# Performance work log

Hardware: AMD Instinct MI355X
Metric: run time of the kernel (lower is better)

## Reference

```python
import jax, jax.numpy as jnp
import numpy as np

# Static configuration (from init_kwargs)
SPLIT_SEC = (128, 320, 320)   # (n_nucl_species..., n_up, n_dn)
N = sum(SPLIT_SEC)            # 768 particles
N_NUCL = sum(SPLIT_SEC[:-2])  # 128
N_DN = SPLIT_SEC[-1]          # 320
SINGLE = 256
PAIR = 64
D_FEAT = SINGLE + len(SPLIT_SEC) * PAIR + len(SPLIT_SEC) * SINGLE  # 1216
SQRT2 = 1.4142135623730951
GELU_RESCALE = 1.7128586      # fvmc rescaled-gelu constant (unit output variance)

_SPLIT_IDX = np.cumsum(SPLIT_SEC)[:-1]

def _pair_type():
    pt = np.zeros((N, N), np.int32)
    sn, se = slice(0, N_NUCL), slice(N_NUCL, N)
    su = slice(N_NUCL, N_NUCL + SPLIT_SEC[-2])
    sd = slice(N_NUCL + SPLIT_SEC[-2], N)
    pt[sn, se] = pt[se, sn] = 1
    pt[su, su] = pt[sd, sd] = 2
    pt[su, sd] = pt[sd, su] = 3
    return pt

PAIR_TYPE = _pair_type()  # static int mask, values in {0,1,2,3}

def actv(x):
    # parse_activation('gelu', rescale=True)
    return jax.nn.gelu(x) * GELU_RESCALE

def residual(x, y):
    # adaptive_residual with rescale=True (shapes always match here)
    return (x + y) / SQRT2

def aggregate_features(h1, h2):
    # per-section mean of h1 over particles -> (n_sec, d1), tiled to (N, n_sec, d1)
    h1_mean = jnp.stack([s.mean(axis=0) for s in jnp.split(h1, _SPLIT_IDX, axis=0)], axis=0)
    h1_mean = jnp.tile(h1_mean[None], (N, 1, 1))
    # per-section mean of h2 over axis 1 -> (N, n_sec, d2)
    h2_mean = jnp.stack([s.mean(axis=1) for s in jnp.split(h2, _SPLIT_IDX, axis=1)], axis=-2)
    # spin symmetry: swap the last two (up/dn) mean channels for the dn rows
    h1_sw = jnp.stack([h1_mean[-N_DN:, -1], h1_mean[-N_DN:, -2]], axis=1)
    h1_mean = h1_mean.at[-N_DN:, -2:].set(h1_sw)
    h2_sw = jnp.stack([h2_mean[-N_DN:, -1], h2_mean[-N_DN:, -2]], axis=1)
    h2_mean = h2_mean.at[-N_DN:, -2:].set(h2_sw)
    return jnp.concatenate([h1, h2_mean.reshape(N, -1), h1_mean.reshape(N, -1)], axis=-1)

def setup_inputs() -> dict:
    key = jax.random.key(0)
    ks = jax.random.split(key, 5)
    sc = lambda fan_in: 1.0 / np.sqrt(fan_in)  # lecun-normal-ish scale
    return {
        "h1": jax.random.normal(ks[0], (N, SINGLE), jnp.float32),
        "h2": jax.random.normal(ks[1], (N, N, PAIR), jnp.float32),
        "W1n": jax.random.normal(ks[2], (D_FEAT, SINGLE), jnp.float32) * sc(D_FEAT),
        "b1n": jnp.zeros((SINGLE,), jnp.float32),
        "W1e": jax.random.normal(ks[3], (D_FEAT, SINGLE), jnp.float32) * sc(D_FEAT),
        "b1e": jnp.zeros((SINGLE,), jnp.float32),
        "W2": jax.random.normal(ks[4], (4, PAIR, PAIR), jnp.float32) * sc(PAIR),
        "b2": jnp.zeros((4, PAIR), jnp.float32),
    }

def reference(h1, h2, W1n, b1n, W1e, b1e, W2, b2):
    feats = aggregate_features(h1, h2)  # (N, D_FEAT)
    # h1 update: separate Dense for nuclei vs electrons
    h1_new = jnp.concatenate([
        feats[:N_NUCL] @ W1n + b1n,
        feats[N_NUCL:] @ W1e + b1e,
    ], axis=0)
    h1_out = residual(h1, actv(h1_new))
    # h2 update: per pair-type Dense, masked scatter back (4 static types)
    pt = jnp.asarray(PAIR_TYPE)
    h2_new = jnp.zeros((N, N, PAIR), h2.dtype)
    for p in range(4):
        mask = (pt == p)[..., None]
        h2_new = h2_new + mask * (jnp.einsum('nmd,de->nme', h2, W2[p]) + b2[p])
    h2_out = residual(h2, actv(h2_new))
    return h1_out, h2_out
```

## Files before the change

### kernel.cpp

```cpp
#include <hip/hip_runtime.h>


#define H1OUT_ELEMS (768 * 256)

typedef short short8 __attribute__((ext_vector_type(8)));
typedef float f32x4 __attribute__((ext_vector_type(4)));

__device__ __forceinline__ unsigned short f2bf(float f) {
    unsigned u = __builtin_bit_cast(unsigned, f);
    unsigned r = u + 0x7fffu + ((u >> 16) & 1u);
    return (unsigned short)(r >> 16);
}

__device__ __forceinline__ float gelu_res(float x, float hv) {
    float x2 = x * x;
    float z = x * fmaf(-0.1029432196f, x2, -2.3025850930f);
    float e = __builtin_amdgcn_exp2f(z);
    float r = __builtin_amdgcn_rcpf(1.f + e);
    return fmaf(x * r, 1.2111740f, hv * 0.70710678f);
}

__global__ __launch_bounds__(256) void k_h2pre(
    const float* __restrict__ h2, const float* __restrict__ W2,
    const float* __restrict__ b2, const float* __restrict__ h1,
    const float* __restrict__ W1n, const float* __restrict__ W1e,
    float* __restrict__ out2, float* __restrict__ part2,
    float* __restrict__ part1, unsigned short* __restrict__ WT) {
    __shared__ union SM {
        struct {
            unsigned short A16[64][72];
            unsigned short BT[64][72];
            float          red[16][68];
        } g;
        float tile[64][65];
    } sm;

    int b = blockIdx.x;
    const int t = threadIdx.x;

    if (b < 12) {
        float s = 0.f;
        #pragma unroll 8
        for (int r = 0; r < 64; ++r) s += h1[(size_t)(b * 64 + r) * 256 + t];
        part1[b * 256 + t] = s;
        return;
    }
    if (b < 164) {
        int idx = b - 12;
        int mtx = idx / 76;
        int r2  = idx % 76;
        int k0 = (r2 / 4) * 64, e0 = (r2 % 4) * 64;
        const float* W = mtx ? W1e : W1n;
        #pragma unroll
        for (int i = 0; i < 16; ++i) {
            int j = i * 256 + t;
            int kr = j >> 6, ec = j & 63;
            sm.tile[kr][ec] = W[(size_t)(k0 + kr) * 256 + e0 + ec];
        }
        __syncthreads();
        #pragma unroll
        for (int i = 0; i < 16; ++i) {
            int j = i * 256 + t;
            int er = j >> 6, kc = j & 63;
            WT[((size_t)mtx * 256 + e0 + er) * 1216 + k0 + kc] = f2bf(sm.tile[kc][er]);
        }
        return;
    }

    b -= 164;
    const int ct = b % 12;
    const int n  = b / 12;
    const int m0 = ct * 64;

    const int rs = (n < 128) ? 0 : ((n < 448) ? 1 : 2);
    const int cs = (ct < 2) ? 0 : ((ct < 7) ? 1 : 2);
    int p;
    if (rs == 0)      p = (cs == 0) ? 0 : 1;
    else if (rs == 1) p = (cs == 0) ? 1 : ((cs == 1) ? 2 : 3);
    else              p = (cs == 0) ? 1 : ((cs == 1) ? 3 : 2);

    const float* src = h2 + ((size_t)n * 768 + m0) * 64;
    const int row0 = t >> 4, c4 = (t & 15) << 2;

    float4 v0 = *reinterpret_cast<const float4*>(src + (row0 +  0) * 64 + c4);
    float4 v1 = *reinterpret_cast<const float4*>(src + (row0 + 16) * 64 + c4);
    float4 v2 = *reinterpret_cast<const float4*>(src + (row0 + 32) * 64 + c4);
    float4 v3 = *reinterpret_cast<const float4*>(src + (row0 + 48) * 64 + c4);

    {
        ushort4 bv;
        bv.x = f2bf(v0.x); bv.y = f2bf(v0.y); bv.z = f2bf(v0.z); bv.w = f2bf(v0.w);
        *reinterpret_cast<ushort4*>(&sm.g.A16[row0][c4]) = bv;
        bv.x = f2bf(v1.x); bv.y = f2bf(v1.y); bv.z = f2bf(v1.z); bv.w = f2bf(v1.w);
        *reinterpret_cast<ushort4*>(&sm.g.A16[row0 + 16][c4]) = bv;
        bv.x = f2bf(v2.x); bv.y = f2bf(v2.y); bv.z = f2bf(v2.z); bv.w = f2bf(v2.w);
        *reinterpret_cast<ushort4*>(&sm.g.A16[row0 + 32][c4]) = bv;
        bv.x = f2bf(v3.x); bv.y = f2bf(v3.y); bv.z = f2bf(v3.z); bv.w = f2bf(v3.w);
        *reinterpret_cast<ushort4*>(&sm.g.A16[row0 + 48][c4]) = bv;
    }
    {
        float4 cs4;
        cs4.x = v0.x + v1.x + v2.x + v3.x;
        cs4.y = v0.y + v1.y + v2.y + v3.y;
        cs4.z = v0.z + v1.z + v2.z + v3.z;
        cs4.w = v0.w + v1.w + v2.w + v3.w;
        *reinterpret_cast<float4*>(&sm.g.red[row0][c4]) = cs4;
    }
    const float* w = W2 + p * 4096;
    #pragma unroll
    for (int i = 0; i < 16; ++i) {
        int idx = i * 256 + t;
        int d = idx >> 6, e = idx & 63;
        sm.g.BT[e][d] = f2bf(w[idx]);
    }
    __syncthreads();

    const int lane = t & 63;
    const int wv = t >> 6;

    if (wv == 0) {
        float s = 0.f;
        #pragma unroll
        for (int r = 0; r < 16; ++r) s += sm.g.red[r][lane];
        part2[((size_t)n * 12 + ct) * 64 + lane] = s;
    }

    const int wm = wv >> 1, we = wv & 1;
    const int lr = lane & 15;
    const int lk = lane >> 4;

    f32x4 acc[2][2] = {};
    #pragma unroll
    for (int kh = 0; kh < 2; ++kh) {
        short8 aF[2], bF[2];
        int k = kh * 32 + lk * 8;
        #pragma unroll
        for (int fm = 0; fm < 2; ++fm)
            aF[fm] = *reinterpret_cast<const short8*>(&sm.g.A16[wm * 32 + fm * 16 + lr][k]);
        #pragma unroll
        for (int fe = 0; fe < 2; ++fe)
            bF[fe] = *reinterpret_cast<const short8*>(&sm.g.BT[we * 32 + fe * 16 + lr][k]);
        #pragma unroll
        for (int fm = 0; fm < 2; ++fm)
            #pragma unroll
            for (int fe = 0; fe < 2; ++fe)
                acc[fm][fe] = __builtin_amdgcn_mfma_f32_16x16x32_bf16(
                    aF[fm], bF[fe], acc[fm][fe], 0, 0, 0);
    }

    float* dst = out2 + ((size_t)n * 768 + m0) * 64;
    #pragma unroll
    for (int fm = 0; fm < 2; ++fm) {
        #pragma unroll
        for (int fe = 0; fe < 2; ++fe) {
            int e = we * 32 + fe * 16 + lr;
            float bias = b2[p * 64 + e];
            #pragma unroll
            for (int r = 0; r < 4; ++r) {
                int m = wm * 32 + fm * 16 + lk * 4 + r;
                float hv = src[m * 64 + e];
                float o = gelu_res(acc[fm][fe][r] + bias, hv);
                __builtin_nontemporal_store(o, dst + m * 64 + e);
            }
        }
    }
}

__global__ __launch_bounds__(256) void k_h1f(
    const float* __restrict__ h1, const unsigned short* __restrict__ WT,
    const float* __restrict__ part2, const float* __restrict__ part1,
    const float* __restrict__ b1n, const float* __restrict__ b1e,
    float* __restrict__ out1) {
    __shared__ unsigned short FL[16][1224];

    const int n0 = blockIdx.x * 16;
    const int half = blockIdx.y;
    const int t = threadIdx.x;
    const bool dn = (n0 >= 448);
    const bool nucl = (n0 < 128);

    #pragma unroll
    for (int i = 0; i < 16; ++i) {
        int idx = i * 256 + t;
        int r = idx >> 8, c = idx & 255;
        FL[r][c] = f2bf(h1[(size_t)(n0 + r) * 256 + c]);
    }
    #pragma unroll
    for (int i = 0; i < 12; ++i) {
        int idx = i * 256 + t;
        int r = idx / 192, c = idx % 192;
        int sec = c >> 6, d = c & 63;
        int s2 = (dn && sec >= 1) ? (3 - sec) : sec;
        const float* pr = part2 + (size_t)(n0 + r) * 768;
        float s;
        if (s2 == 0) {
            s = (pr[d] + pr[64 + d]) * (1.f / 128.f);
        } else {
            int q0 = (s2 == 1) ? 2 : 7;
            s = 0.f;
            #pragma unroll
            for (int q = 0; q < 5; ++q) s += pr[(q0 + q) * 64 + d];
            s *= (1.f / 320.f);
        }
        FL[r][256 + c] = f2bf(s);
    }
    #pragma unroll
    for (int i = 0; i < 3; ++i) {
        int j = i * 256 + t;
        int sec = j >> 8, e2 = j & 255;
        int s2 = (dn && sec >= 1) ? (3 - sec) : sec;
        float s;
        if (s2 == 0) {
            s = (part1[e2] + part1[256 + e2]) * (1.f / 128.f);
        } else {
            int q0 = (s2 == 1) ? 2 : 7;
            s = 0.f;
            #pragma unroll
            for (int q = 0; q < 5; ++q) s += part1[(q0 + q) * 256 + e2];
            s *= (1.f / 320.f);
        }
        unsigned short bv = f2bf(s);
        #pragma unroll
        for (int r = 0; r < 16; ++r) FL[r][448 + j] = bv;
    }
    __syncthreads();

    const int w = t >> 6, lane = t & 63;
    const int lr = lane & 15, lk = lane >> 4;
    const int e0 = half * 128 + w * 32;
    const unsigned short* BT = WT + (nucl ? 0 : (size_t)256 * 1216);
    const unsigned short* br0 = BT + (size_t)(e0 + lr) * 1216 + lk * 8;
    const unsigned short* br1 = br0 + (size_t)16 * 1216;
    const unsigned short* ar = &FL[lr][lk * 8];

    f32x4 acc0 = {}, acc1 = {};
    #pragma unroll 2
    for (int k = 0; k < 1216; k += 32) {
        short8 aF = *reinterpret_cast<const short8*>(ar + k);
        short8 b0 = *reinterpret_cast<const short8*>(br0 + k);
        short8 b1 = *reinterpret_cast<const short8*>(br1 + k);
        acc0 = __builtin_amdgcn_mfma_f32_16x16x32_bf16(aF, b0, acc0, 0, 0, 0);
        acc1 = __builtin_amdgcn_mfma_f32_16x16x32_bf16(aF, b1, acc1, 0, 0, 0);
    }

    const float* bb = nucl ? b1n : b1e;
    #pragma unroll
    for (int j = 0; j < 2; ++j) {
        const f32x4 a = j ? acc1 : acc0;
        int e = e0 + j * 16 + lr;
        float bias = bb[e];
        #pragma unroll
        for (int r = 0; r < 4; ++r) {
            int m = n0 + lk * 4 + r;
            float hv = h1[(size_t)m * 256 + e];
            out1[(size_t)m * 256 + e] = gelu_res(a[r] + bias, hv);
        }
    }
}

extern "C" void kernel_launch(void* const* d_in, const int* in_sizes, int n_in,
                              void* d_out, int out_size, void* d_ws, size_t ws_size,
                              hipStream_t stream) {
    const float* h1  = (const float*)d_in[0];
    const float* h2  = (const float*)d_in[1];
    const float* W1n = (const float*)d_in[2];
    const float* b1n = (const float*)d_in[3];
    const float* W1e = (const float*)d_in[4];
    const float* b1e = (const float*)d_in[5];
    const float* W2  = (const float*)d_in[6];
    const float* b2  = (const float*)d_in[7];

    float* out1 = (float*)d_out;
    float* out2 = out1 + H1OUT_ELEMS;

    float* part2 = (float*)d_ws;
    float* part1 = part2 + 768 * 12 * 64;
    unsigned short* WT = (unsigned short*)(part1 + 12 * 256);

    k_h2pre<<<dim3(164 + 12 * 768), 256, 0, stream>>>(
        h2, W2, b2, h1, W1n, W1e, out2, part2, part1, WT);
    k_h1f<<<dim3(48, 2), 256, 0, stream>>>(h1, WT, part2, part1, b1n, b1e, out1);
}
```

Measured before the change: 86.28 us.

## Load MFMA fragments directly from global memory and vectorize weight transpose

The h2 tile blocks no longer stage h2 and W2 through LDS as bf16. Each wave reads its MFMA A and B fragments straight from global memory and converts them to bf16 in registers, and LDS is kept only for the column-sum reduction, which now runs after the MFMA. The W1 transpose blocks switch to 64x32 tiles with 16-byte vectorized bf16 stores, which doubles the number of those blocks. This cuts LDS use and moves the barrier later, at the cost of redundant global loads: each A fragment is loaded by two waves and each W2 fragment is gathered with strided scalar loads in every block.

```diff
diff --git a/kernel.cpp b/kernel.cpp
--- a/kernel.cpp
+++ b/kernel.cpp
@@ -27,12 +27,8 @@
     float* __restrict__ out2, float* __restrict__ part2,
     float* __restrict__ part1, unsigned short* __restrict__ WT) {
     __shared__ union SM {
-        struct {
-            unsigned short A16[64][72];
-            unsigned short BT[64][72];
-            float          red[16][68];
-        } g;
-        float tile[64][65];
+        float red[2][16][68];
+        float tile2[64][33];
     } sm;
 
     int b = blockIdx.x;
@@ -45,29 +41,29 @@
         part1[b * 256 + t] = s;
         return;
     }
-    if (b < 164) {
+    if (b < 316) {
         int idx = b - 12;
-        int mtx = idx / 76;
-        int r2  = idx % 76;
-        int k0 = (r2 / 4) * 64, e0 = (r2 % 4) * 64;
+        int mtx = idx / 152;
+        int r2  = idx % 152;
+        int k0 = (r2 >> 3) * 64, e0 = (r2 & 7) * 32;
         const float* W = mtx ? W1e : W1n;
         #pragma unroll
-        for (int i = 0; i < 16; ++i) {
+        for (int i = 0; i < 8; ++i) {
             int j = i * 256 + t;
-            int kr = j >> 6, ec = j & 63;
-            sm.tile[kr][ec] = W[(size_t)(k0 + kr) * 256 + e0 + ec];
+            int kr = j >> 5, ec = j & 31;
+            sm.tile2[kr][ec] = W[(size_t)(k0 + kr) * 256 + e0 + ec];
         }
         __syncthreads();
-        #pragma unroll
-        for (int i = 0; i < 16; ++i) {
-            int j = i * 256 + t;
-            int er = j >> 6, kc = j & 63;
-            WT[((size_t)mtx * 256 + e0 + er) * 1216 + k0 + kc] = f2bf(sm.tile[kc][er]);
-        }
+        int er = t >> 3, k8 = (t & 7) * 8;
+        short8 o;
+        #pragma unroll
+        for (int j = 0; j < 8; ++j) o[j] = (short)f2bf(sm.tile2[k8 + j][er]);
+        *reinterpret_cast<short8*>(
+            &WT[((size_t)mtx * 256 + e0 + er) * 1216 + k0 + k8]) = o;
         return;
     }
 
-    b -= 164;
+    b -= 316;
     const int ct = b % 12;
     const int n  = b / 12;
     const int m0 = ct * 64;
@@ -80,72 +76,86 @@
     else              p = (cs == 0) ? 1 : ((cs == 1) ? 3 : 2);
 
     const float* src = h2 + ((size_t)n * 768 + m0) * 64;
-    const int row0 = t >> 4, c4 = (t & 15) << 2;
-
-    float4 v0 = *reinterpret_cast<const float4*>(src + (row0 +  0) * 64 + c4);
-    float4 v1 = *reinterpret_cast<const float4*>(src + (row0 + 16) * 64 + c4);
-    float4 v2 = *reinterpret_cast<const float4*>(src + (row0 + 32) * 64 + c4);
-    float4 v3 = *reinterpret_cast<const float4*>(src + (row0 + 48) * 64 + c4);
-
-    {
-        ushort4 bv;
-        bv.x = f2bf(v0.x); bv.y = f2bf(v0.y); bv.z = f2bf(v0.z); bv.w = f2bf(v0.w);
-        *reinterpret_cast<ushort4*>(&sm.g.A16[row0][c4]) = bv;
-        bv.x = f2bf(v1.x); bv.y = f2bf(v1.y); bv.z = f2bf(v1.z); bv.w = f2bf(v1.w);
-        *reinterpret_cast<ushort4*>(&sm.g.A16[row0 + 16][c4]) = bv;
-        bv.x = f2bf(v2.x); bv.y = f2bf(v2.y); bv.z = f2bf(v2.z); bv.w = f2bf(v2.w);
-        *reinterpret_cast<ushort4*>(&sm.g.A16[row0 + 32][c4]) = bv;
-        bv.x = f2bf(v3.x); bv.y = f2bf(v3.y); bv.z = f2bf(v3.z); bv.w = f2bf(v3.w);
-        *reinterpret_cast<ushort4*>(&sm.g.A16[row0 + 48][c4]) = bv;
-    }
-    {
-        float4 cs4;
-        cs4.x = v0.x + v1.x + v2.x + v3.x;
-        cs4.y = v0.y + v1.y + v2.y + v3.y;
-        cs4.z = v0.z + v1.z + v2.z + v3.z;
-        cs4.w = v0.w + v1.w + v2.w + v3.w;
-        *reinterpret_cast<float4*>(&sm.g.red[row0][c4]) = cs4;
-    }
-    const float* w = W2 + p * 4096;
-    #pragma unroll
-    for (int i = 0; i < 16; ++i) {
-        int idx = i * 256 + t;
-        int d = idx >> 6, e = idx & 63;
-        sm.g.BT[e][d] = f2bf(w[idx]);
-    }
-    __syncthreads();
-
     const int lane = t & 63;
     const int wv = t >> 6;
-
-    if (wv == 0) {
-        float s = 0.f;
-        #pragma unroll
-        for (int r = 0; r < 16; ++r) s += sm.g.red[r][lane];
-        part2[((size_t)n * 12 + ct) * 64 + lane] = s;
-    }
-
     const int wm = wv >> 1, we = wv & 1;
-    const int lr = lane & 15;
-    const int lk = lane >> 4;
+    const int lr = lane & 15, lk = lane >> 4;
+
+    const float* arow = src + (wm * 32 + lr) * 64 + lk * 8;
+    float4 af[2][2][2];
+    #pragma unroll
+    for (int fm = 0; fm < 2; ++fm)
+        #pragma unroll
+        for (int kh = 0; kh < 2; ++kh) {
+            const float* pp = arow + fm * 1024 + kh * 32;
+            af[fm][kh][0] = *reinterpret_cast<const float4*>(pp);
+            af[fm][kh][1] = *reinterpret_cast<const float4*>(pp + 4);
+        }
+
+    if (we == 0) {
+        #pragma unroll
+        for (int kh = 0; kh < 2; ++kh) {
+            float4 s0, s1;
+            s0.x = af[0][kh][0].x + af[1][kh][0].x;
+            s0.y = af[0][kh][0].y + af[1][kh][0].y;
+            s0.z = af[0][kh][0].z + af[1][kh][0].z;
+            s0.w = af[0][kh][0].w + af[1][kh][0].w;
+            s1.x = af[0][kh][1].x + af[1][kh][1].x;
+            s1.y = af[0][kh][1].y + af[1][kh][1].y;
+            s1.z = af[0][kh][1].z + af[1][kh][1].z;
+            s1.w = af[0][kh][1].w + af[1][kh][1].w;
+            *reinterpret_cast<float4*>(&sm.red[wm][lr][kh * 32 + lk * 8]) = s0;
+            *reinterpret_cast<float4*>(&sm.red[wm][lr][kh * 32 + lk * 8 + 4]) = s1;
+        }
+    }
+
+    short8 aF[2][2];
+    #pragma unroll
+    for (int fm = 0; fm < 2; ++fm)
+        #pragma unroll
+        for (int kh = 0; kh < 2; ++kh) {
+            short8 o;
+            o[0] = (short)f2bf(af[fm][kh][0].x);
+            o[1] = (short)f2bf(af[fm][kh][0].y);
+            o[2] = (short)f2bf(af[fm][kh][0].z);
+            o[3] = (short)f2bf(af[fm][kh][0].w);
+            o[4] = (short)f2bf(af[fm][kh][1].x);
+            o[5] = (short)f2bf(af[fm][kh][1].y);
+            o[6] = (short)f2bf(af[fm][kh][1].z);
+            o[7] = (short)f2bf(af[fm][kh][1].w);
+            aF[fm][kh] = o;
+        }
+
+    const float* wp = W2 + p * 4096 + we * 32 + lr;
+    short8 bF[2][2];
+    #pragma unroll
+    for (int fe = 0; fe < 2; ++fe)
+        #pragma unroll
+        for (int kh = 0; kh < 2; ++kh) {
+            const float* q = wp + fe * 16 + (kh * 32 + lk * 8) * 64;
+            short8 o;
+            #pragma unroll
+            for (int j = 0; j < 8; ++j) o[j] = (short)f2bf(q[j * 64]);
+            bF[fe][kh] = o;
+        }
 
     f32x4 acc[2][2] = {};
     #pragma unroll
-    for (int kh = 0; kh < 2; ++kh) {
-        short8 aF[2], bF[2];
-        int k = kh * 32 + lk * 8;
-        #pragma unroll
-        for (int fm = 0; fm < 2; ++fm)
-            aF[fm] = *reinterpret_cast<const short8*>(&sm.g.A16[wm * 32 + fm * 16 + lr][k]);
-        #pragma unroll
-        for (int fe = 0; fe < 2; ++fe)
-            bF[fe] = *reinterpret_cast<const short8*>(&sm.g.BT[we * 32 + fe * 16 + lr][k]);
+    for (int kh = 0; kh < 2; ++kh)
         #pragma unroll
         for (int fm = 0; fm < 2; ++fm)
             #pragma unroll
             for (int fe = 0; fe < 2; ++fe)
                 acc[fm][fe] = __builtin_amdgcn_mfma_f32_16x16x32_bf16(
-                    aF[fm], bF[fe], acc[fm][fe], 0, 0, 0);
+                    aF[fm][kh], bF[fe][kh], acc[fm][fe], 0, 0, 0);
+
+    __syncthreads();
+
+    if (t < 64) {
+        float s = 0.f;
+        #pragma unroll
+        for (int r = 0; r < 16; ++r) s += sm.red[0][r][t] + sm.red[1][r][t];
+        part2[((size_t)n * 12 + ct) * 64 + t] = s;
     }
 
     float* dst = out2 + ((size_t)n * 768 + m0) * 64;
@@ -277,7 +287,7 @@
     float* part1 = part2 + 768 * 12 * 64;
     unsigned short* WT = (unsigned short*)(part1 + 12 * 256);
 
-    k_h2pre<<<dim3(164 + 12 * 768), 256, 0, stream>>>(
+    k_h2pre<<<dim3(316 + 12 * 768), 256, 0, stream>>>(
         h2, W2, b2, h1, W1n, W1e, out2, part2, part1, WT);
     k_h1f<<<dim3(48, 2), 256, 0, stream>>>(h1, WT, part2, part1, b1n, b1e, out1);
 }
```

After: 82.30 us. 1.05x faster.
